# Kernel tuning notes

Measured on AMD Instinct MI355X. Metric: run time of the kernel, lower is better.

## Reference

```python
import jax, jax.numpy as jnp
import numpy as np

B, T, A, C, H = 8, 50, 38, 64, 1024
IN = A * A * C + A * A  # 93860


def setup_inputs() -> dict:
    key = jax.random.key(0)
    ks = jax.random.split(key, 10)
    s = 0.02  # small init so gates do not instantly saturate
    return {
        "tensors": jax.random.normal(ks[0], (B, T, A, A, C), dtype=jnp.float32),
        "masks": jax.random.uniform(ks[1], (B, T, A * A), dtype=jnp.float32),
        "W_ih": jax.random.normal(ks[2], (4 * H, IN), dtype=jnp.float32) * s,
        "W_hh": jax.random.normal(ks[3], (4 * H, H), dtype=jnp.float32) * s,
        "b_ih": jax.random.normal(ks[4], (4 * H,), dtype=jnp.float32) * s,
        "b_hh": jax.random.normal(ks[5], (4 * H,), dtype=jnp.float32) * s,
        "W_att": jax.random.normal(ks[6], (A * A, H), dtype=jnp.float32) * s,
        "b_att": jax.random.normal(ks[7], (A * A,), dtype=jnp.float32) * s,
        "W_out": jax.random.normal(ks[8], (A * A, H), dtype=jnp.float32) * s,
        "b_out": jax.random.normal(ks[9], (A * A,), dtype=jnp.float32) * s,
    }


def reference(tensors, masks, W_ih, W_hh, b_ih, b_hh, W_att, b_att, W_out, b_out):
    b = tensors.shape[0]
    h_dim = W_hh.shape[1]
    a = int(np.sqrt(W_att.shape[0]))

    def step(carry, xs):
        h, c, att = carry
        x_t, m_t = xs  # x_t: (B,A,A,C), m_t: (B,A*A)
        gated = x_t * att[..., None]                      # attention-gated input
        inp = jnp.concatenate([gated.reshape(b, -1), m_t], axis=1)  # (B, IN)
        gates = inp @ W_ih.T + b_ih + h @ W_hh.T + b_hh   # (B, 4H)
        i_g, f_g, g_g, o_g = jnp.split(gates, 4, axis=1)  # torch LSTMCell order
        i_g = jax.nn.sigmoid(i_g)
        f_g = jax.nn.sigmoid(f_g)
        g_g = jnp.tanh(g_g)
        o_g = jax.nn.sigmoid(o_g)
        c_new = f_g * c + i_g * g_g
        h_new = o_g * jnp.tanh(c_new)
        h_relu = jax.nn.relu(h_new)
        att_new = jax.nn.sigmoid(h_relu @ W_att.T + b_att).reshape(b, a, a)
        out_t = h_relu @ W_out.T + b_out
        return (h_new, c_new, att_new), out_t

    init = (
        jnp.zeros((b, h_dim), jnp.float32),
        jnp.zeros((b, h_dim), jnp.float32),
        jnp.zeros((b, a, a), jnp.float32),
    )
    xs = (jnp.swapaxes(tensors, 0, 1), jnp.swapaxes(masks, 0, 1))  # time-major
    _, outs = jax.lax.scan(step, init, xs)                          # (T,B,A*A)
    out = jnp.swapaxes(outs, 0, 1)                                  # (B,T,A*A)
    return jax.nn.sigmoid(out)  # eval-mode branch (not self.training)
```

## Files before the change

kernel.cpp:

```cpp
#include <hip/hip_runtime.h>
#include <hip/hip_fp16.h>
#include <math.h>

#define BB 8
#define TT 50
#define AA 1444
#define HH 1024
#define G4 4096
#define INX 92416
#define IND 93860
#define INDP 93888
#define NKB 2934
#define SEG 16
#define SEGSZ 91

typedef unsigned int u32;
typedef unsigned short u16;
typedef u32 u32x4 __attribute__((ext_vector_type(4)));
typedef short s16x8 __attribute__((ext_vector_type(8)));
typedef float f32x4 __attribute__((ext_vector_type(4)));

__device__ __forceinline__ float sigf(float x) { return 1.0f / (1.0f + expf(-x)); }

__device__ __forceinline__ u16 f2bf(float f) {
    u32 u = __float_as_uint(f);
    u = (u + 0x7FFFu + ((u >> 16) & 1u)) >> 16;
    return (u16)u;
}
__device__ __forceinline__ u16 f2h(float f) { return __half_as_ushort(__float2half(f)); }
__device__ __forceinline__ float h2f(u16 h) { return __half2float(__ushort_as_half(h)); }

__global__ void k_init(float* __restrict__ h, float* __restrict__ c0,
                       float* __restrict__ c1, float* __restrict__ att) {
    int i = blockIdx.x * 256 + threadIdx.x;
    if (i < BB * HH) { h[i] = 0.f; c0[i] = 0.f; c1[i] = 0.f; }
    if (i < BB * AA) att[i] = 0.f;
}

__global__ __launch_bounds__(256)
void k_cvtswz(const float* __restrict__ W, u16* __restrict__ Wf) {
    const size_t idx = (size_t)blockIdx.x * 256 + threadIdx.x;
    const int l = (int)(idx & 63);
    const size_t mkb = idx >> 6;
    const int kb = (int)(mkb % NKB);
    const int m = (int)(mkb / NKB);
    const int row = m * 16 + (l & 15);
    const int k0 = kb * 32 + ((l >> 4) << 3);
    union { u16 s[8]; u32x4 v; } pk;
    if (k0 + 8 <= IND) {
        const float* src = W + (size_t)row * IND + k0;
        float4 a = *(const float4*)src;
        float4 b = *(const float4*)(src + 4);
        pk.s[0] = f2bf(a.x); pk.s[1] = f2bf(a.y);
        pk.s[2] = f2bf(a.z); pk.s[3] = f2bf(a.w);
        pk.s[4] = f2bf(b.x); pk.s[5] = f2bf(b.y);
        pk.s[6] = f2bf(b.z); pk.s[7] = f2bf(b.w);
    } else {
#pragma unroll
        for (int j = 0; j < 8; ++j) {
            const int k = k0 + j;
            pk.s[j] = (k < IND) ? f2bf(W[(size_t)row * IND + k]) : (u16)0;
        }
    }
    *(u32x4*)(Wf + idx * 8) = pk.v;
}

__global__ __launch_bounds__(512)
void k_gm(const float* __restrict__ W, const float* __restrict__ masks,
          float* __restrict__ gm) {
    const int g0 = blockIdx.x * 8;
    const int n = threadIdx.x;
    if (n >= BB * TT) return;
    const int b = n & 7, t = n >> 3;
    const float* mp = masks + ((size_t)b * TT + t) * AA;
    const float* wr[8];
#pragma unroll
    for (int r = 0; r < 8; ++r) wr[r] = W + (size_t)(g0 + r) * IND + INX;
    float acc[8];
#pragma unroll
    for (int r = 0; r < 8; ++r) acc[r] = 0.f;
    for (int k = 0; k < AA; ++k) {
        const float mv = mp[k];
#pragma unroll
        for (int r = 0; r < 8; ++r) acc[r] = fmaf(wr[r][k], mv, acc[r]);
    }
#pragma unroll
    for (int r = 0; r < 8; ++r)
        gm[((size_t)t * BB + b) * G4 + g0 + r] = acc[r];
}

__global__ __launch_bounds__(256)
void k_pre(const u16* __restrict__ Wf, const float* __restrict__ x,
           u16* __restrict__ Y) {
    const int ij = blockIdx.x >> 4;
    const int gc = blockIdx.x & 15;
    const int tid = threadIdx.x;
    const int w = tid >> 6, l = tid & 63;
    __shared__ u16 xs[1024];
    __shared__ u16 os[4096];
    char* xsb = (char*)xs;
    char* osb = (char*)os;

    s16x8 a[4][2];
#pragma unroll
    for (int q = 0; q < 4; ++q) {
        const size_t m = (size_t)gc * 16 + w * 4 + q;
#pragma unroll
        for (int kb = 0; kb < 2; ++kb)
            a[q][kb] = __builtin_nontemporal_load(
                (const s16x8*)(Wf + (m * NKB + (size_t)ij * 2 + kb) * 512 + l * 8));
    }

    const int scol = tid >> 4, scg = tid & 15;
    for (int nt = 0; nt < 25; ++nt) {
        {
            const int n = nt * 16 + scol;
            const int b = n & 7, t = n >> 3;
            float4 v = *(const float4*)(x + (((size_t)b * TT + t) * AA + ij) * 64 + scg * 4);
            u32 lo = ((u32)f2bf(v.y) << 16) | f2bf(v.x);
            u32 hi = ((u32)f2bf(v.w) << 16) | f2bf(v.z);
            const int addr = (scol * 128 + scg * 8) ^ ((scol & 7) << 4);
            *(u32*)(xsb + addr) = lo;
            *(u32*)(xsb + addr + 4) = hi;
        }
        __syncthreads();
        f32x4 acc[4];
        {
            const int col = l & 15;
            const int c0b = (l >> 4) * 16;
            const int swz = (col & 7) << 4;
            s16x8 b0 = *(const s16x8*)(xsb + ((col * 128 + c0b) ^ swz));
            s16x8 b1 = *(const s16x8*)(xsb + ((col * 128 + 64 + c0b) ^ swz));
#pragma unroll
            for (int q = 0; q < 4; ++q) {
                acc[q] = (f32x4){0.f, 0.f, 0.f, 0.f};
                acc[q] = __builtin_amdgcn_mfma_f32_16x16x32_bf16(a[q][0], b0, acc[q], 0, 0, 0);
                acc[q] = __builtin_amdgcn_mfma_f32_16x16x32_bf16(a[q][1], b1, acc[q], 0, 0, 0);
            }
        }
        {
            const int nrow = l & 15;
            const int swz = (nrow & 7) << 4;
#pragma unroll
            for (int q = 0; q < 4; ++q) {
                u32 lo = ((u32)f2h(acc[q][1]) << 16) | f2h(acc[q][0]);
                u32 hi = ((u32)f2h(acc[q][3]) << 16) | f2h(acc[q][2]);
                const int addr = (nrow * 512 + w * 128 + q * 32 + (l >> 4) * 8) ^ swz;
                *(u32*)(osb + addr) = lo;
                *(u32*)(osb + addr + 4) = hi;
            }
        }
        __syncthreads();
        {
            const int n = nt * 16 + scol;
            const int b = n & 7, t = n >> 3;
            const int swz = (scol & 7) << 4;
            u32x4 d0 = *(const u32x4*)(osb + ((scol * 512 + scg * 32) ^ swz));
            u32x4 d1 = *(const u32x4*)(osb + ((scol * 512 + scg * 32 + 16) ^ swz));
            u16* yp = Y + (((size_t)t * AA + ij) * BB + b) * G4 + gc * 256 + scg * 16;
            *(u32x4*)yp = d0;
            *(u32x4*)(yp + 8) = d1;
        }
        __syncthreads();
    }
}

__global__ __launch_bounds__(512)
void k_contract(const u16* __restrict__ Y, const float* __restrict__ att,
                const float* __restrict__ Whh, const float* __restrict__ h,
                float* __restrict__ part, float* __restrict__ gates2, int t) {
    const int w = threadIdx.x >> 6, l = threadIdx.x & 63;
    if (blockIdx.x < 128) {
        const int b = blockIdx.x >> 4, seg = blockIdx.x & 15;
        const int g0 = threadIdx.x * 8;
        const int ij0 = seg * SEGSZ;
        const int ij1 = min(ij0 + SEGSZ, AA);
        float acc[8];
#pragma unroll
        for (int k = 0; k < 8; ++k) acc[k] = 0.f;
        const u16* yp = Y + (((size_t)t * AA + ij0) * BB + b) * G4 + g0;
        const float* ap = att + b * AA;
        for (int ij = ij0; ij < ij1; ++ij, yp += (size_t)BB * G4) {
            const float am = ap[ij];
            u32x4 v = *(const u32x4*)yp;
            const u16* vs = (const u16*)&v;
#pragma unroll
            for (int k = 0; k < 8; ++k)
                acc[k] = fmaf(am, h2f(vs[k]), acc[k]);
        }
        float* pp = part + ((size_t)seg * BB + b) * G4 + g0;
#pragma unroll
        for (int k = 0; k < 8; ++k) pp[k] = acc[k];
    } else {
        const int g0 = (blockIdx.x - 128) * 16 + w * 2;
        float acc[2][8];
#pragma unroll
        for (int r = 0; r < 2; ++r)
#pragma unroll
            for (int b = 0; b < 8; ++b) acc[r][b] = 0.f;
#pragma unroll 4
        for (int i = 0; i < 16; ++i) {
            const int j = l + 64 * i;
            float hv[8];
#pragma unroll
            for (int b = 0; b < 8; ++b) hv[b] = h[b * HH + j];
#pragma unroll
            for (int r = 0; r < 2; ++r) {
                const float w0 = Whh[(size_t)(g0 + r) * HH + j];
#pragma unroll
                for (int b = 0; b < 8; ++b) acc[r][b] = fmaf(w0, hv[b], acc[r][b]);
            }
        }
#pragma unroll
        for (int r = 0; r < 2; ++r)
#pragma unroll
            for (int b = 0; b < 8; ++b) {
                float v = acc[r][b];
                for (int off = 32; off; off >>= 1) v += __shfl_down(v, off, 64);
                if (l == 0) gates2[b * G4 + g0 + r] = v;
            }
    }
}

__global__ __launch_bounds__(512)
void k_cell3(const float* __restrict__ part, const float* __restrict__ gm,
             const float* __restrict__ gates2, const float* __restrict__ bih,
             const float* __restrict__ bhh, const float* __restrict__ c_in,
             float* __restrict__ c_out, float* __restrict__ h,
             float* __restrict__ hrelu, int t) {
    const int i = blockIdx.x * 512 + threadIdx.x;
    const int b = i >> 10, j = i & (HH - 1);
    float g[4];
#pragma unroll
    for (int r = 0; r < 4; ++r) {
        const int gg = r * HH + j;
        float s = 0.f;
#pragma unroll
        for (int sg = 0; sg < SEG; ++sg)
            s += part[((size_t)sg * BB + b) * G4 + gg];
        g[r] = s + gm[((size_t)t * BB + b) * G4 + gg] + gates2[b * G4 + gg]
             + bih[gg] + bhh[gg];
    }
    const float ig = sigf(g[0]);
    const float fg = sigf(g[1]);
    const float gv = tanhf(g[2]);
    const float og = sigf(g[3]);
    const float cn = fg * c_in[i] + ig * gv;
    const float hn = og * tanhf(cn);
    c_out[i] = cn;
    h[i] = hn;
    hrelu[i] = fmaxf(hn, 0.f);
}

__global__ __launch_bounds__(512)
void k_post2(const float* __restrict__ hrelu,
             const float* __restrict__ Watt, const float* __restrict__ batt,
             const float* __restrict__ Wout, const float* __restrict__ bout,
             float* __restrict__ att, float* __restrict__ out, int t) {
    __shared__ float hr[BB][HH];
    for (int i = threadIdx.x; i < BB * HH; i += 512)
        hr[i >> 10][i & (HH - 1)] = hrelu[i];
    __syncthreads();
    const int w = threadIdx.x >> 6, l = threadIdx.x & 63;
    const bool isOut = blockIdx.x < 181;
    if (!isOut && t + 1 >= TT) return;
    const int row = (isOut ? blockIdx.x : (blockIdx.x - 181)) * 8 + w;
    if (row >= AA) return;
    const float* W = isOut ? Wout : Watt;
    float acc[8];
#pragma unroll
    for (int b = 0; b < 8; ++b) acc[b] = 0.f;
#pragma unroll 4
    for (int i = 0; i < 16; ++i) {
        const int j = l + 64 * i;
        const float w0 = W[(size_t)row * HH + j];
#pragma unroll
        for (int b = 0; b < 8; ++b) acc[b] = fmaf(w0, hr[b][j], acc[b]);
    }
#pragma unroll
    for (int b = 0; b < 8; ++b) {
        float v = acc[b];
        for (int off = 32; off; off >>= 1) v += __shfl_xor(v, off, 64);
        acc[b] = v;
    }
    if (l < 8) {
        if (isOut)
            out[((size_t)l * TT + t) * AA + row] = sigf(acc[l] + bout[row]);
        else
            att[l * AA + row] = sigf(acc[l] + batt[row]);
    }
}

__global__ __launch_bounds__(256, 2)
void k_gates_f32(const float* __restrict__ x, const float* __restrict__ masks,
                 const float* __restrict__ Wih, const float* __restrict__ Whh,
                 const float* __restrict__ bih, const float* __restrict__ bhh,
                 const float* __restrict__ h, const float* __restrict__ att,
                 float* __restrict__ gates, int t) {
    __shared__ float att_s[BB * AA];
    const int tid = threadIdx.x;
    for (int i = tid; i < BB * AA; i += 256) att_s[i] = att[i];
    __syncthreads();
    const int g0 = blockIdx.x * 8;
    float acc[8][8];
#pragma unroll
    for (int r = 0; r < 8; ++r)
#pragma unroll
        for (int b = 0; b < 8; ++b) acc[r][b] = 0.f;
    const float* xb = x + (size_t)t * INX;
    for (int k = tid; k < INX; k += 256) {
        const int ij = k >> 6;
        float xa[8];
#pragma unroll
        for (int b = 0; b < 8; ++b)
            xa[b] = xb[(size_t)b * TT * INX + k] * att_s[b * AA + ij];
#pragma unroll
        for (int r = 0; r < 8; ++r) {
            float w = __builtin_nontemporal_load(&Wih[(size_t)(g0 + r) * IND + k]);
#pragma unroll
            for (int b = 0; b < 8; ++b) acc[r][b] = fmaf(w, xa[b], acc[r][b]);
        }
    }
    const float* mb = masks + (size_t)t * AA;
    for (int k = tid; k < AA; k += 256) {
        float mv[8];
#pragma unroll
        for (int b = 0; b < 8; ++b) mv[b] = mb[(size_t)b * TT * AA + k];
#pragma unroll
        for (int r = 0; r < 8; ++r) {
            float w = __builtin_nontemporal_load(&Wih[(size_t)(g0 + r) * IND + INX + k]);
#pragma unroll
            for (int b = 0; b < 8; ++b) acc[r][b] = fmaf(w, mv[b], acc[r][b]);
        }
    }
    for (int j = tid; j < HH; j += 256) {
        float hv[8];
#pragma unroll
        for (int b = 0; b < 8; ++b) hv[b] = h[b * HH + j];
#pragma unroll
        for (int r = 0; r < 8; ++r) {
            float w = Whh[(size_t)(g0 + r) * HH + j];
#pragma unroll
            for (int b = 0; b < 8; ++b) acc[r][b] = fmaf(w, hv[b], acc[r][b]);
        }
    }
#pragma unroll
    for (int r = 0; r < 8; ++r)
#pragma unroll
        for (int b = 0; b < 8; ++b) {
            float v = acc[r][b];
            for (int off = 32; off; off >>= 1) v += __shfl_down(v, off, 64);
            acc[r][b] = v;
        }
    __shared__ float red[4][8][8];
    const int wave = tid >> 6, lane = tid & 63;
    if (lane == 0) {
#pragma unroll
        for (int r = 0; r < 8; ++r)
#pragma unroll
            for (int b = 0; b < 8; ++b) red[wave][r][b] = acc[r][b];
    }
    __syncthreads();
    if (tid < 64) {
        const int r = tid >> 3, b = tid & 7;
        const int g = g0 + r;
        float v = red[0][r][b] + red[1][r][b] + red[2][r][b] + red[3][r][b];
        gates[b * G4 + g] = v + bih[g] + bhh[g];
    }
}

__global__ void k_cell(const float* __restrict__ gates, float* __restrict__ c,
                       float* __restrict__ h, float* __restrict__ hrelu) {
    int idx = blockIdx.x * 256 + threadIdx.x;
    if (idx >= BB * HH) return;
    const int b = idx >> 10, j = idx & (HH - 1);
    const float* gb = gates + b * G4;
    float ig = sigf(gb[j]);
    float fg = sigf(gb[HH + j]);
    float gg = tanhf(gb[2 * HH + j]);
    float og = sigf(gb[3 * HH + j]);
    float cn = fg * c[idx] + ig * gg;
    float hn = og * tanhf(cn);
    c[idx] = cn;
    h[idx] = hn;
    hrelu[idx] = fmaxf(hn, 0.f);
}

__global__ __launch_bounds__(256)
void k_attout(const float* __restrict__ hrelu,
              const float* __restrict__ Watt, const float* __restrict__ batt,
              const float* __restrict__ Wout, const float* __restrict__ bout,
              float* __restrict__ att, float* __restrict__ out, int t) {
    const int wid = blockIdx.x * 4 + (threadIdx.x >> 6);
    const int lane = threadIdx.x & 63;
    if (wid >= 2 * AA) return;
    const bool isAtt = wid < AA;
    const int row = isAtt ? wid : wid - AA;
    const float* W = isAtt ? Watt : Wout;
    float acc[8];
#pragma unroll
    for (int b = 0; b < 8; ++b) acc[b] = 0.f;
    for (int j = lane; j < HH; j += 64) {
        const float w = W[(size_t)row * HH + j];
#pragma unroll
        for (int b = 0; b < 8; ++b) acc[b] = fmaf(w, hrelu[b * HH + j], acc[b]);
    }
#pragma unroll
    for (int b = 0; b < 8; ++b) {
        float v = acc[b];
        for (int off = 32; off; off >>= 1) v += __shfl_xor(v, off, 64);
        acc[b] = v;
    }
    if (lane < 8) {
        const int b = lane;
        if (isAtt)
            att[b * AA + row] = sigf(acc[b] + batt[row]);
        else
            out[((size_t)b * TT + t) * AA + row] = sigf(acc[b] + bout[row]);
    }
}

extern "C" void kernel_launch(void* const* d_in, const int* in_sizes, int n_in,
                              void* d_out, int out_size, void* d_ws, size_t ws_size,
                              hipStream_t stream) {
    const float* tensors = (const float*)d_in[0];
    const float* masks   = (const float*)d_in[1];
    const float* Wih     = (const float*)d_in[2];
    const float* Whh     = (const float*)d_in[3];
    const float* bih     = (const float*)d_in[4];
    const float* bhh     = (const float*)d_in[5];
    const float* Watt    = (const float*)d_in[6];
    const float* batt    = (const float*)d_in[7];
    const float* Wout    = (const float*)d_in[8];
    const float* bout    = (const float*)d_in[9];
    float* out = (float*)d_out;

    float* ws     = (float*)d_ws;
    float* h      = ws;
    float* c0     = h + BB * HH;
    float* c1     = c0 + BB * HH;
    float* hrelu  = c1 + BB * HH;
    float* gates2 = hrelu + BB * HH;
    float* att    = gates2 + BB * G4;
    float* part   = att + BB * AA;
    float* gm     = part + (size_t)SEG * BB * G4;
    u16*   Wf     = (u16*)(gm + (size_t)TT * BB * G4);
    u16*   Y      = Wf + (size_t)G4 * INDP;

    const size_t f32_cnt = (size_t)(4 * BB * HH + BB * G4 + BB * AA)
                         + (size_t)SEG * BB * G4 + (size_t)TT * BB * G4;
    const size_t need = f32_cnt * 4 + (size_t)G4 * INDP * 2
                      + (size_t)TT * AA * BB * G4 * 2;
    const bool fast_path = ws_size >= need;

    k_init<<<46, 256, 0, stream>>>(h, c0, c1, att);
    if (fast_path) {
        k_cvtswz<<<NKB * 64, 256, 0, stream>>>(Wih, Wf);
        k_gm<<<512, 512, 0, stream>>>(Wih, masks, gm);
        k_pre<<<AA * 16, 256, 0, stream>>>(Wf, tensors, Y);
        for (int t = 0; t < TT; ++t) {
            float* cin  = (t & 1) ? c1 : c0;
            float* cout = (t & 1) ? c0 : c1;
            k_contract<<<384, 512, 0, stream>>>(Y, att, Whh, h, part, gates2, t);
            k_cell3<<<16, 512, 0, stream>>>(part, gm, gates2, bih, bhh, cin,
                                            cout, h, hrelu, t);
            k_post2<<<362, 512, 0, stream>>>(hrelu, Watt, batt, Wout, bout,
                                             att, out, t);
        }
    } else {
        for (int t = 0; t < TT; ++t) {
            k_gates_f32<<<512, 256, 0, stream>>>(tensors, masks, Wih, Whh, bih,
                                                 bhh, h, att, part, t);
            k_cell<<<32, 256, 0, stream>>>(part, c0, h, hrelu);
            k_attout<<<722, 256, 0, stream>>>(hrelu, Watt, batt, Wout, bout,
                                              att, out, t);
        }
    }
}
```

Measured before the change: 5.326 ms.

## Fuse W_ih bf16 conversion into k_pre and make Y batch-innermost for contraction

Removes the separate k_cvtswz pass that wrote a swizzled bf16 copy of W_ih; k_pre now loads fp32 weights directly and converts them to bf16 in registers. The Y intermediate is relaid out with the 8 batch values innermost per gate, so each k_contract thread reads one 16-byte vector covering all batches for a gate. k_contract is also split into 64 segments x 8 gate chunks, with attention values staged in shared memory and nontemporal loads. This removes a full weight conversion pass and makes the per-step Y reads more contiguous. In exchange k_pre reads twice as many weight bytes, and k_cell3 has to sum over more partial segments.

```diff
diff --git a/kernel.cpp b/kernel.cpp
--- a/kernel.cpp
+++ b/kernel.cpp
@@ -9,10 +9,7 @@
 #define G4 4096
 #define INX 92416
 #define IND 93860
-#define INDP 93888
-#define NKB 2934
-#define SEG 16
-#define SEGSZ 91
+#define SEG 64
 
 typedef unsigned int u32;
 typedef unsigned short u16;
@@ -35,34 +32,6 @@
     int i = blockIdx.x * 256 + threadIdx.x;
     if (i < BB * HH) { h[i] = 0.f; c0[i] = 0.f; c1[i] = 0.f; }
     if (i < BB * AA) att[i] = 0.f;
-}
-
-__global__ __launch_bounds__(256)
-void k_cvtswz(const float* __restrict__ W, u16* __restrict__ Wf) {
-    const size_t idx = (size_t)blockIdx.x * 256 + threadIdx.x;
-    const int l = (int)(idx & 63);
-    const size_t mkb = idx >> 6;
-    const int kb = (int)(mkb % NKB);
-    const int m = (int)(mkb / NKB);
-    const int row = m * 16 + (l & 15);
-    const int k0 = kb * 32 + ((l >> 4) << 3);
-    union { u16 s[8]; u32x4 v; } pk;
-    if (k0 + 8 <= IND) {
-        const float* src = W + (size_t)row * IND + k0;
-        float4 a = *(const float4*)src;
-        float4 b = *(const float4*)(src + 4);
-        pk.s[0] = f2bf(a.x); pk.s[1] = f2bf(a.y);
-        pk.s[2] = f2bf(a.z); pk.s[3] = f2bf(a.w);
-        pk.s[4] = f2bf(b.x); pk.s[5] = f2bf(b.y);
-        pk.s[6] = f2bf(b.z); pk.s[7] = f2bf(b.w);
-    } else {
-#pragma unroll
-        for (int j = 0; j < 8; ++j) {
-            const int k = k0 + j;
-            pk.s[j] = (k < IND) ? f2bf(W[(size_t)row * IND + k]) : (u16)0;
-        }
-    }
-    *(u32x4*)(Wf + idx * 8) = pk.v;
 }
 
 __global__ __launch_bounds__(512)
@@ -90,25 +59,34 @@
 }
 
 __global__ __launch_bounds__(256)
-void k_pre(const u16* __restrict__ Wf, const float* __restrict__ x,
+void k_pre(const float* __restrict__ W, const float* __restrict__ x,
            u16* __restrict__ Y) {
     const int ij = blockIdx.x >> 4;
     const int gc = blockIdx.x & 15;
     const int tid = threadIdx.x;
     const int w = tid >> 6, l = tid & 63;
     __shared__ u16 xs[1024];
-    __shared__ u16 os[4096];
+    __shared__ u16 os2[4096];
     char* xsb = (char*)xs;
-    char* osb = (char*)os;
+    char* osb = (char*)os2;
 
     s16x8 a[4][2];
 #pragma unroll
     for (int q = 0; q < 4; ++q) {
-        const size_t m = (size_t)gc * 16 + w * 4 + q;
-#pragma unroll
-        for (int kb = 0; kb < 2; ++kb)
-            a[q][kb] = __builtin_nontemporal_load(
-                (const s16x8*)(Wf + (m * NKB + (size_t)ij * 2 + kb) * 512 + l * 8));
+        const int grow = gc * 256 + (w * 4 + q) * 16 + (l & 15);
+#pragma unroll
+        for (int kb = 0; kb < 2; ++kb) {
+            const size_t off = (size_t)grow * IND + (size_t)ij * 64 + kb * 32
+                             + ((l >> 4) << 3);
+            f32x4 v0 = __builtin_nontemporal_load((const f32x4*)(W + off));
+            f32x4 v1 = __builtin_nontemporal_load((const f32x4*)(W + off + 4));
+            union { u16 s[8]; s16x8 v; } pk;
+            pk.s[0] = f2bf(v0[0]); pk.s[1] = f2bf(v0[1]);
+            pk.s[2] = f2bf(v0[2]); pk.s[3] = f2bf(v0[3]);
+            pk.s[4] = f2bf(v1[0]); pk.s[5] = f2bf(v1[1]);
+            pk.s[6] = f2bf(v1[2]); pk.s[7] = f2bf(v1[3]);
+            a[q][kb] = pk.v;
+        }
     }
 
     const int scol = tid >> 4, scg = tid & 15;
@@ -116,9 +94,9 @@
         {
             const int n = nt * 16 + scol;
             const int b = n & 7, t = n >> 3;
-            float4 v = *(const float4*)(x + (((size_t)b * TT + t) * AA + ij) * 64 + scg * 4);
-            u32 lo = ((u32)f2bf(v.y) << 16) | f2bf(v.x);
-            u32 hi = ((u32)f2bf(v.w) << 16) | f2bf(v.z);
+            f32x4 v = *(const f32x4*)(x + (((size_t)b * TT + t) * AA + ij) * 64 + scg * 4);
+            u32 lo = ((u32)f2bf(v[1]) << 16) | f2bf(v[0]);
+            u32 hi = ((u32)f2bf(v[3]) << 16) | f2bf(v[2]);
             const int addr = (scol * 128 + scg * 8) ^ ((scol & 7) << 4);
             *(u32*)(xsb + addr) = lo;
             *(u32*)(xsb + addr + 4) = hi;
@@ -139,27 +117,31 @@
             }
         }
         {
-            const int nrow = l & 15;
-            const int swz = (nrow & 7) << 4;
+            const int n = l & 15;
+            const int tl = n >> 3, bcol = n & 7;
 #pragma unroll
             for (int q = 0; q < 4; ++q) {
-                u32 lo = ((u32)f2h(acc[q][1]) << 16) | f2h(acc[q][0]);
-                u32 hi = ((u32)f2h(acc[q][3]) << 16) | f2h(acc[q][2]);
-                const int addr = (nrow * 512 + w * 128 + q * 32 + (l >> 4) * 8) ^ swz;
-                *(u32*)(osb + addr) = lo;
-                *(u32*)(osb + addr + 4) = hi;
+                const int gb = (w * 4 + q) * 16 + ((l >> 4) << 2);
+#pragma unroll
+                for (int i = 0; i < 4; ++i) {
+                    const int g = gb + i;
+                    const int addr = tl * 4096
+                                   + ((g * 16 + bcol * 2) ^ (((g >> 3) & 7) << 4));
+                    *(u16*)(osb + addr) = f2h(acc[q][i]);
+                }
             }
         }
         __syncthreads();
         {
-            const int n = nt * 16 + scol;
-            const int b = n & 7, t = n >> 3;
-            const int swz = (scol & 7) << 4;
-            u32x4 d0 = *(const u32x4*)(osb + ((scol * 512 + scg * 32) ^ swz));
-            u32x4 d1 = *(const u32x4*)(osb + ((scol * 512 + scg * 32 + 16) ^ swz));
-            u16* yp = Y + (((size_t)t * AA + ij) * BB + b) * G4 + gc * 256 + scg * 16;
-            *(u32x4*)yp = d0;
-            *(u32x4*)(yp + 8) = d1;
+            const int gl = tid;
+#pragma unroll
+            for (int tl = 0; tl < 2; ++tl) {
+                const int t = nt * 2 + tl;
+                const int addr = tl * 4096 + ((gl * 16) ^ (((gl >> 3) & 7) << 4));
+                u32x4 d = *(const u32x4*)(osb + addr);
+                __builtin_nontemporal_store(d,
+                    (u32x4*)(Y + (((size_t)t * AA + ij) * G4 + gc * 256 + gl) * 8));
+            }
         }
         __syncthreads();
     }
@@ -170,29 +152,48 @@
                 const float* __restrict__ Whh, const float* __restrict__ h,
                 float* __restrict__ part, float* __restrict__ gates2, int t) {
     const int w = threadIdx.x >> 6, l = threadIdx.x & 63;
-    if (blockIdx.x < 128) {
-        const int b = blockIdx.x >> 4, seg = blockIdx.x & 15;
-        const int g0 = threadIdx.x * 8;
-        const int ij0 = seg * SEGSZ;
-        const int ij1 = min(ij0 + SEGSZ, AA);
+    if (blockIdx.x < 512) {
+        const int seg = blockIdx.x >> 3, gch = blockIdx.x & 7;
+        const int ij0 = (seg * AA) >> 6, ij1 = ((seg + 1) * AA) >> 6;
+        const int nij = ij1 - ij0;
+        const int g = gch * 512 + threadIdx.x;
+        __shared__ float atts[8][24];
+        if (threadIdx.x < nij) {
+#pragma unroll
+            for (int b = 0; b < 8; ++b)
+                atts[b][threadIdx.x] = att[b * AA + ij0 + threadIdx.x];
+        }
+        __syncthreads();
         float acc[8];
 #pragma unroll
-        for (int k = 0; k < 8; ++k) acc[k] = 0.f;
-        const u16* yp = Y + (((size_t)t * AA + ij0) * BB + b) * G4 + g0;
-        const float* ap = att + b * AA;
-        for (int ij = ij0; ij < ij1; ++ij, yp += (size_t)BB * G4) {
-            const float am = ap[ij];
-            u32x4 v = *(const u32x4*)yp;
-            const u16* vs = (const u16*)&v;
-#pragma unroll
-            for (int k = 0; k < 8; ++k)
-                acc[k] = fmaf(am, h2f(vs[k]), acc[k]);
-        }
-        float* pp = part + ((size_t)seg * BB + b) * G4 + g0;
-#pragma unroll
-        for (int k = 0; k < 8; ++k) pp[k] = acc[k];
+        for (int b = 0; b < 8; ++b) acc[b] = 0.f;
+        const u16* yp = Y + (((size_t)t * AA + ij0) * G4 + g) * 8;
+        int k = 0;
+        for (; k + 2 <= nij; k += 2) {
+            u32x4 v0 = __builtin_nontemporal_load((const u32x4*)yp);
+            u32x4 v1 = __builtin_nontemporal_load((const u32x4*)(yp + (size_t)G4 * 8));
+            const u16* s0 = (const u16*)&v0;
+            const u16* s1 = (const u16*)&v1;
+#pragma unroll
+            for (int b = 0; b < 8; ++b)
+                acc[b] = fmaf(atts[b][k], h2f(s0[b]), acc[b]);
+#pragma unroll
+            for (int b = 0; b < 8; ++b)
+                acc[b] = fmaf(atts[b][k + 1], h2f(s1[b]), acc[b]);
+            yp += (size_t)2 * G4 * 8;
+        }
+        if (k < nij) {
+            u32x4 v0 = __builtin_nontemporal_load((const u32x4*)yp);
+            const u16* s0 = (const u16*)&v0;
+#pragma unroll
+            for (int b = 0; b < 8; ++b)
+                acc[b] = fmaf(atts[b][k], h2f(s0[b]), acc[b]);
+        }
+        float* pp = part + ((size_t)seg * G4 + g) * 8;
+#pragma unroll
+        for (int b = 0; b < 8; ++b) pp[b] = acc[b];
     } else {
-        const int g0 = (blockIdx.x - 128) * 16 + w * 2;
+        const int g0 = (blockIdx.x - 512) * 16 + w * 2;
         float acc[2][8];
 #pragma unroll
         for (int r = 0; r < 2; ++r)
@@ -235,9 +236,8 @@
     for (int r = 0; r < 4; ++r) {
         const int gg = r * HH + j;
         float s = 0.f;
-#pragma unroll
         for (int sg = 0; sg < SEG; ++sg)
-            s += part[((size_t)sg * BB + b) * G4 + gg];
+            s += part[((size_t)sg * G4 + gg) * 8 + b];
         g[r] = s + gm[((size_t)t * BB + b) * G4 + gg] + gates2[b * G4 + gg]
              + bih[gg] + bhh[gg];
     }
@@ -443,25 +443,22 @@
     float* gates2 = hrelu + BB * HH;
     float* att    = gates2 + BB * G4;
     float* part   = att + BB * AA;
-    float* gm     = part + (size_t)SEG * BB * G4;
-    u16*   Wf     = (u16*)(gm + (size_t)TT * BB * G4);
-    u16*   Y      = Wf + (size_t)G4 * INDP;
+    float* gm     = part + (size_t)SEG * G4 * BB;
+    u16*   Y      = (u16*)(gm + (size_t)TT * BB * G4);
 
     const size_t f32_cnt = (size_t)(4 * BB * HH + BB * G4 + BB * AA)
-                         + (size_t)SEG * BB * G4 + (size_t)TT * BB * G4;
-    const size_t need = f32_cnt * 4 + (size_t)G4 * INDP * 2
-                      + (size_t)TT * AA * BB * G4 * 2;
+                         + (size_t)SEG * G4 * BB + (size_t)TT * BB * G4;
+    const size_t need = f32_cnt * 4 + (size_t)TT * AA * G4 * BB * 2;
     const bool fast_path = ws_size >= need;
 
     k_init<<<46, 256, 0, stream>>>(h, c0, c1, att);
     if (fast_path) {
-        k_cvtswz<<<NKB * 64, 256, 0, stream>>>(Wih, Wf);
         k_gm<<<512, 512, 0, stream>>>(Wih, masks, gm);
-        k_pre<<<AA * 16, 256, 0, stream>>>(Wf, tensors, Y);
+        k_pre<<<AA * 16, 256, 0, stream>>>(Wih, tensors, Y);
         for (int t = 0; t < TT; ++t) {
             float* cin  = (t & 1) ? c1 : c0;
             float* cout = (t & 1) ? c0 : c1;
-            k_contract<<<384, 512, 0, stream>>>(Y, att, Whh, h, part, gates2, t);
+            k_contract<<<768, 512, 0, stream>>>(Y, att, Whh, h, part, gates2, t);
             k_cell3<<<16, 512, 0, stream>>>(part, gm, gates2, bih, bhh, cin,
                                             cout, h, hrelu, t);
             k_post2<<<362, 512, 0, stream>>>(hrelu, Watt, batt, Wout, bout,
```

Measured after the change: 6.305 ms. +18.4%, slower.
